# Performance work log

Hardware: AMD Instinct MI355X
Metric: run time of the kernel (lower is better)

The kernel has to match this reference:

```python
import jax, jax.numpy as jnp
import numpy as np
import math

BS, L, DIM, H = 2, 1024, 1024, 16
DPH = DIM // H            # 64 dim per head
PHI_DIM = DPH * 1         # phi_size_ratio = 1
N_PROJS = 200
MIN_LOG_STD = math.log(1e-5)
SQRT_PHI = math.sqrt(PHI_DIM)


def setup_inputs() -> dict:
    key = jax.random.key(0)
    ks = jax.random.split(key, 8)
    lin = lambda k: jax.random.normal(k, (DIM, DIM), jnp.float32) * 0.02
    return {
        "x": jax.random.normal(ks[0], (BS, L, DIM), jnp.float32),
        "mask": jnp.ones((BS, L), dtype=jnp.bool_),
        "Wq": lin(ks[1]), "bq": jnp.zeros((DIM,), jnp.float32),
        "Wk": lin(ks[2]), "bk": jnp.zeros((DIM,), jnp.float32),
        "Wv": lin(ks[3]), "bv": jnp.zeros((DIM,), jnp.float32),
        "Wo": lin(ks[4]), "bo": jnp.zeros((DIM,), jnp.float32),
        "log_sigma": jnp.zeros((H, 1, DPH), jnp.float32),  # log(1.0) init
        "random_projs": jax.random.normal(ks[5], (N_PROJS, PHI_DIM, DPH), jnp.float32),
    }


def _phi(x, rp_scaled):
    # x: (b, l, h, d); rp_scaled: (h, phi, d). arccos features: relu(proj) / sqrt(phi_dim)
    x = x / jnp.maximum(jnp.linalg.norm(x, axis=-1, keepdims=True), 1e-12)
    px = jnp.einsum('blhd,hpd->blhp', x, rp_scaled)
    return jax.nn.relu(px) / SQRT_PHI


def _causal_rfa(phi_q, phi_k, v):
    # sequential S,z recurrence, time-major scan
    def step(carry, inp):
        S, z = carry
        pk, pq, vt = inp                       # (b,h,phi),(b,h,phi),(b,h,d)
        S = S + pk[..., :, None] * vt[..., None, :]
        z = z + pk
        num = jnp.einsum('bhp,bhpd->bhd', pq, S)
        den = jnp.einsum('bhp,bhp->bh', pq, z)
        return (S, z), num / jnp.maximum(den, 1e-5)[..., None]

    S0 = jnp.zeros((BS, H, PHI_DIM, DPH), jnp.float32)
    z0 = jnp.zeros((BS, H, PHI_DIM), jnp.float32)
    xs = (jnp.transpose(phi_k, (1, 0, 2, 3)),
          jnp.transpose(phi_q, (1, 0, 2, 3)),
          jnp.transpose(v, (1, 0, 2, 3)))
    _, h_t = jax.lax.scan(step, (S0, z0), xs)  # (l, b, h, d)
    return jnp.transpose(h_t, (1, 0, 2, 3))     # (b, l, h, d)


def reference(x, mask, Wq, bq, Wk, bk, Wv, bv, Wo, bo, log_sigma, random_projs):
    q = (x @ Wq.T + bq).reshape(BS, L, H, DPH)
    k = (x @ Wk.T + bk).reshape(BS, L, H, DPH)
    v = (x @ Wv.T + bv).reshape(BS, L, H, DPH)
    # eval mode: proj_id = 0 for every head
    scale = jnp.exp(jnp.maximum(log_sigma, MIN_LOG_STD))                  # (h,1,d)
    rp = scale * jnp.broadcast_to(random_projs[0], (H, PHI_DIM, DPH))     # (h,phi,d)
    phi_q = _phi(q, rp)
    phi_k = _phi(k, rp) * mask[:, :, None, None].astype(jnp.float32)
    h = _causal_rfa(phi_q, phi_k, v)                                      # (b,l,h,d)
    return h.reshape(BS, L, DIM) @ Wo.T + bo
```

## Files before the change

### kernel.cpp

```cpp
#include <hip/hip_runtime.h>


typedef unsigned short ushort_t;
typedef unsigned long long u64_t;
typedef __attribute__((ext_vector_type(8))) __bf16 bf16x8;
typedef __attribute__((ext_vector_type(4))) float f32x4;

#define MLS -11.512925464970229f

__device__ __forceinline__ ushort_t f2b(float f) {
  union { float f; unsigned u; } v; v.f = f;
  unsigned r = v.u + 0x7FFFu + ((v.u >> 16) & 1u);
  return (ushort_t)(r >> 16);
}

__device__ __forceinline__ void gload16(const void* g, void* l) {
  __builtin_amdgcn_global_load_lds((__attribute__((address_space(1))) void*)(void*)g,
                                   (__attribute__((address_space(3))) void*)l, 16, 0, 0);
}

__device__ __forceinline__ f32x4 mfma_bf16(bf16x8 a, bf16x8 b, f32x4 c) {
  return __builtin_amdgcn_mfma_f32_16x16x32_bf16(a, b, c, 0, 0, 0);
}

__global__ __launch_bounds__(256) void convert_kernel(
    const float* __restrict__ x, const float* __restrict__ Wq, const float* __restrict__ Wk,
    const float* __restrict__ Wv, const float* __restrict__ Wo,
    const float* __restrict__ bq, const float* __restrict__ bk, const float* __restrict__ bv,
    const float* __restrict__ lsig, const float* __restrict__ rp0,
    ushort_t* __restrict__ xb, ushort_t* __restrict__ Wcat, ushort_t* __restrict__ Wob,
    float* __restrict__ bcat, float* __restrict__ sclbuf, ushort_t* __restrict__ rpb) {
  const size_t NX = (size_t)1 << 21, NW = (size_t)1 << 20;
  const size_t nch = (NX + 4 * NW) >> 3;
  size_t stride = (size_t)gridDim.x * 256;
  for (size_t i = (size_t)blockIdx.x * 256 + threadIdx.x; i < nch + 1024; i += stride) {
    if (i < nch) {
      size_t e = i << 3;
      const float* src; ushort_t* dst;
      if (e < NX)            { src = x  + e;               dst = xb   + e; }
      else if (e < NX + NW)  { src = Wq + (e - NX);        dst = Wcat + (e - NX); }
      else if (e < NX + 2*NW){ src = Wk + (e - NX - NW);   dst = Wcat + (e - NX); }
      else if (e < NX + 3*NW){ src = Wv + (e - NX - 2*NW); dst = Wcat + (e - NX); }
      else                   { src = Wo + (e - NX - 3*NW); dst = Wob  + (e - NX - 3*NW); }
      float4 a = *(const float4*)src, c = *(const float4*)(src + 4);
      uint4 u;
      u.x = (unsigned)f2b(a.x) | ((unsigned)f2b(a.y) << 16);
      u.y = (unsigned)f2b(a.z) | ((unsigned)f2b(a.w) << 16);
      u.z = (unsigned)f2b(c.x) | ((unsigned)f2b(c.y) << 16);
      u.w = (unsigned)f2b(c.z) | ((unsigned)f2b(c.w) << 16);
      *(uint4*)dst = u;
    } else {
      int j = (int)(i - nch);
      sclbuf[j] = expf(fmaxf(lsig[j], MLS));
      bcat[j] = bq[j]; bcat[1024 + j] = bk[j]; bcat[2048 + j] = bv[j];
#pragma unroll
      for (int jj = 0; jj < 4; ++jj) {
        int pe = j * 4 + jj;
        rpb[pe] = f2b(rp0[pe]);
      }
    }
  }
}

__global__ __launch_bounds__(512, 2) void qkvphi_kernel(
    const ushort_t* __restrict__ A, const ushort_t* __restrict__ Bm,
    const float* __restrict__ bias, const float* __restrict__ sclbuf,
    const ushort_t* __restrict__ rpb,
    ushort_t* __restrict__ phiq, ushort_t* __restrict__ phik, ushort_t* __restrict__ vbT,
    float* __restrict__ Sg, float* __restrict__ zg) {
  __shared__ __align__(16) ushort_t smem[40960];
  const int K = 1024;
  int blk = blockIdx.x;
  int hg = blk & 15, by = blk >> 4;
  int m0 = by << 7;
  int tid = threadIdx.x;
  int w = tid >> 6, l = tid & 63;
  int wr = w & 3, wc = w >> 2;
  int lr = l & 15, lg = l >> 4;
  bf16x8 rpf[2][4];
#pragma unroll
  for (int kk = 0; kk < 2; ++kk)
#pragma unroll
    for (int ni = 0; ni < 4; ++ni)
      rpf[kk][ni] = *(const bf16x8*)(rpb + (ni*16 + lr)*64 + kk*32 + lg*8);

  f32x4 acc[2][6] = {};
  auto stage = [&](int buf, int k0) {
    ushort_t* Ad = smem + buf*8192;
    ushort_t* Bd = smem + 16384 + buf*12288;
#pragma unroll
    for (int it = 0; it < 2; ++it) {
      int idx = it*512 + tid, row = idx >> 3, cg = idx & 7;
      gload16(A + (size_t)(m0 + row)*K + k0 + ((cg ^ (row & 7)) << 3), Ad + idx*8);
    }
#pragma unroll
    for (int it = 0; it < 3; ++it) {
      int idx = it*512 + tid, row = idx >> 3, cg = idx & 7;
      int grow = (row >> 6)*1024 + hg*64 + (row & 63);
      gload16(Bm + (size_t)grow*K + k0 + ((cg ^ (row & 7)) << 3), Bd + idx*8);
    }
  };
  auto compute = [&](int buf) {
    const ushort_t* Ab = smem + buf*8192;
    const ushort_t* Bb = smem + 16384 + buf*12288;
#pragma unroll
    for (int kk = 0; kk < 2; ++kk) {
      bf16x8 af[2], bfr[6];
#pragma unroll
      for (int ii = 0; ii < 2; ++ii) {
        int r = wr*32 + ii*16 + lr;
        af[ii] = *(const bf16x8*)(Ab + r*64 + (((kk*4 + lg) ^ (r & 7)) << 3));
      }
#pragma unroll
      for (int ii = 0; ii < 6; ++ii) {
        int brow = (ii < 4) ? (wc*64 + ii*16 + lr) : (128 + wc*32 + (ii - 4)*16 + lr);
        bfr[ii] = *(const bf16x8*)(Bb + brow*64 + (((kk*4 + lg) ^ (brow & 7)) << 3));
      }
#pragma unroll
      for (int mi = 0; mi < 2; ++mi)
#pragma unroll
        for (int ni = 0; ni < 6; ++ni)
          acc[mi][ni] = mfma_bf16(af[mi], bfr[ni], acc[mi][ni]);
    }
  };
  stage(0, 0);
  for (int t = 0; t < 15; ++t) {
    stage((t + 1) & 1, (t + 1) * 64);
    asm volatile("s_waitcnt vmcnt(5)" ::: "memory");
    __builtin_amdgcn_s_barrier();
    compute(t & 1);
    asm volatile("s_waitcnt lgkmcnt(0)" ::: "memory");
    __builtin_amdgcn_s_barrier();
  }
  asm volatile("s_waitcnt vmcnt(0)" ::: "memory");
  __builtin_amdgcn_s_barrier();
  compute(1);
  __syncthreads();

  int b = m0 >> 10, tloc0 = m0 & 1023;
  int kt = tloc0 >> 7;
  size_t hbase = ((size_t)(b*16 + hg) << 16);
  {
    ushort_t* Vt = smem + 16384;
    float bv2[2];
#pragma unroll
    for (int j = 0; j < 2; ++j) bv2[j] = bias[2048 + hg*64 + wc*32 + j*16 + lr];
#pragma unroll
    for (int mi = 0; mi < 2; ++mi) {
      int lloc0 = wr*32 + mi*16 + lg*4;
#pragma unroll
      for (int j = 0; j < 2; ++j) {
        int d = wc*32 + j*16 + lr;
        u64_t u = 0;
#pragma unroll
        for (int r = 0; r < 4; ++r)
          u |= (u64_t)f2b(acc[mi][4 + j][r] + bv2[j]) << (16*r);
        int sv0 = (lloc0 & 7) | ((((lloc0 >> 3) ^ (d & 15)) & 15) << 3);
        *(u64_t*)(Vt + d*128 + sv0) = u;
      }
    }
  }
  ushort_t* Ys = smem + w*2048;
  {
    float bias4[4], scl4[4];
#pragma unroll
    for (int ni = 0; ni < 4; ++ni) {
      bias4[ni] = bias[wc*1024 + hg*64 + ni*16 + lr];
      scl4[ni]  = sclbuf[hg*64 + ni*16 + lr];
    }
#pragma unroll
    for (int mi = 0; mi < 2; ++mi) {
      float v4[4][4];
      float ss[4] = {0.f, 0.f, 0.f, 0.f};
#pragma unroll
      for (int ni = 0; ni < 4; ++ni)
#pragma unroll
        for (int r = 0; r < 4; ++r) {
          float vv = acc[mi][ni][r] + bias4[ni];
          v4[ni][r] = vv;
          ss[r] += vv * vv;
        }
#pragma unroll
      for (int r = 0; r < 4; ++r) {
        float s = ss[r];
        s += __shfl_xor(s, 1); s += __shfl_xor(s, 2);
        s += __shfl_xor(s, 4); s += __shfl_xor(s, 8);
        ss[r] = 1.f / fmaxf(sqrtf(s), 1e-12f);
      }
#pragma unroll
      for (int ni = 0; ni < 4; ++ni) {
        int c = ni*16 + lr;
#pragma unroll
        for (int r = 0; r < 4; ++r) {
          int rl = mi*16 + lg*4 + r;
          Ys[rl*64 + (((c >> 3) ^ (rl & 7)) << 3) + (c & 7)] = f2b(v4[ni][r] * ss[r] * scl4[ni]);
        }
      }
    }
  }
  {
    ushort_t* dst = wc ? phik : phiq;
    ushort_t* KT = smem + 28672;
    float* zpart = (float*)(smem + 36864);
    f32x4 acc2[2][4] = {};
#pragma unroll
    for (int kk = 0; kk < 2; ++kk) {
      bf16x8 af2[2];
#pragma unroll
      for (int mi = 0; mi < 2; ++mi) {
        int rl = mi*16 + lr;
        af2[mi] = *(const bf16x8*)(Ys + rl*64 + (((kk*4 + lg) ^ (rl & 7)) << 3));
      }
#pragma unroll
      for (int mi = 0; mi < 2; ++mi)
#pragma unroll
        for (int ni = 0; ni < 4; ++ni)
          acc2[mi][ni] = mfma_bf16(af2[mi], rpf[kk][ni], acc2[mi][ni]);
    }
    ushort_t* Pt = Ys;
    float zp[4] = {0.f, 0.f, 0.f, 0.f};
#pragma unroll
    for (int mi = 0; mi < 2; ++mi)
#pragma unroll
      for (int ni = 0; ni < 4; ++ni) {
        u64_t ku = 0;
#pragma unroll
        for (int r = 0; r < 4; ++r) {
          int rl = mi*16 + lg*4 + r;
          int p = ni*16 + lr;
          float val = fmaxf(acc2[mi][ni][r], 0.f) * 0.125f;
          ushort_t uv = f2b(val);
          int sp = (p & 7) | ((((p >> 3) ^ (rl & 7)) & 7) << 3);
          Pt[rl*64 + sp] = uv;
          ku |= (u64_t)uv << (16*r);
          zp[ni] += val;
        }
        if (wc) {
          int lloc0 = wr*32 + mi*16 + lg*4;
          int p = ni*16 + lr;
          int sv0 = (lloc0 & 7) | ((((lloc0 >> 3) ^ (p & 15)) & 15) << 3);
          *(u64_t*)(KT + p*128 + sv0) = ku;
        }
      }
    if (wc) {
#pragma unroll
      for (int ni = 0; ni < 4; ++ni) {
        float s = zp[ni];
        s += __shfl_xor(s, 16); s += __shfl_xor(s, 32);
        if (lg == 0) zpart[wr*64 + ni*16 + lr] = s;
      }
    }
    size_t gp = hbase + (size_t)(tloc0 + wr*32)*64;
#pragma unroll
    for (int ii = 0; ii < 4; ++ii) {
      int chunk = ii*64 + l;
      uint4 u = *(const uint4*)(Pt + chunk*8);
      *(uint4*)(dst + gp + chunk*8) = u;
    }
  }
  __syncthreads();
  if (wc == 0) {
    const ushort_t* Vt = smem + 16384;
    const ushort_t* KT = smem + 28672;
    f32x4 sacc[4] = {};
#pragma unroll
    for (int kk = 0; kk < 4; ++kk) {
      int p = wr*16 + lr;
      bf16x8 af = *(const bf16x8*)(KT + p*128 + (((kk*4 + lg) ^ (p & 15)) << 3));
#pragma unroll
      for (int ni = 0; ni < 4; ++ni) {
        int d = ni*16 + lr;
        bf16x8 bfv = *(const bf16x8*)(Vt + d*128 + (((kk*4 + lg) ^ (d & 15)) << 3));
        sacc[ni] = mfma_bf16(af, bfv, sacc[ni]);
      }
    }
    float* Sb = Sg + (((size_t)(b*16 + hg))*8 + kt)*4096;
#pragma unroll
    for (int ni = 0; ni < 4; ++ni)
#pragma unroll
      for (int r = 0; r < 4; ++r)
        Sb[(wr*16 + lg*4 + r)*64 + ni*16 + lr] = sacc[ni][r];
  } else if (w == 4) {
    const float* zpart = (const float*)(smem + 36864);
    float s = zpart[l & 63] + zpart[64 + (l & 63)] + zpart[128 + (l & 63)] + zpart[192 + (l & 63)];
    zg[(((size_t)(b*16 + hg))*8 + kt)*64 + (l & 63)] = s;
  }
  {
    const ushort_t* Vt = smem + 16384;
#pragma unroll
    for (int c = tid; c < 1024; c += 512) {
      int d = c >> 4, off = c & 15;
      uint4 u = *(const uint4*)(Vt + c*8);
      *(uint4*)(vbT + hbase + (size_t)d*1024 + kt*128 + off*8) = u;
    }
  }
}

__global__ __launch_bounds__(256) void outproj_kernel(
    const ushort_t* __restrict__ A, const ushort_t* __restrict__ Bm,
    const float* __restrict__ bias, float* __restrict__ C) {
  __shared__ __align__(16) ushort_t smem[16384];
  const int K = 1024;
  int wid = (blockIdx.x & 7) * 64 + (blockIdx.x >> 3);
  int bx = wid & 15, by = wid >> 4;
  int m0 = by << 6, n0 = bx << 6;
  int tid = threadIdx.x, w = tid >> 6, l = tid & 63;
  int lr = l & 15, lg = l >> 4;
  auto stage = [&](int buf, int k0) {
    ushort_t* Ad = smem + buf*4096;
    ushort_t* Bd = smem + 8192 + buf*4096;
#pragma unroll
    for (int it = 0; it < 2; ++it) {
      int idx = it*256 + tid, row = idx >> 3, cg = idx & 7;
      gload16(A + (size_t)(m0 + row)*K + k0 + ((cg ^ (row & 7)) << 3), Ad + idx*8);
    }
#pragma unroll
    for (int it = 0; it < 2; ++it) {
      int idx = it*256 + tid, row = idx >> 3, cg = idx & 7;
      gload16(Bm + (size_t)(n0 + row)*K + k0 + ((cg ^ (row & 7)) << 3), Bd + idx*8);
    }
  };
  f32x4 acc[4] = {};
  auto compute = [&](int buf) {
    const ushort_t* Ab = smem + buf*4096;
    const ushort_t* Bb = smem + 8192 + buf*4096;
#pragma unroll
    for (int kk = 0; kk < 2; ++kk) {
      int ra = w*16 + lr;
      bf16x8 af = *(const bf16x8*)(Ab + ra*64 + (((kk*4 + lg) ^ (ra & 7)) << 3));
      bf16x8 bfr[4];
#pragma unroll
      for (int i = 0; i < 4; ++i) {
        int rb = i*16 + lr;
        bfr[i] = *(const bf16x8*)(Bb + rb*64 + (((kk*4 + lg) ^ (rb & 7)) << 3));
      }
#pragma unroll
      for (int ni = 0; ni < 4; ++ni)
        acc[ni] = mfma_bf16(af, bfr[ni], acc[ni]);
    }
  };
  stage(0, 0);
  for (int t = 0; t < 15; ++t) {
    stage((t + 1) & 1, (t + 1) * 64);
    asm volatile("s_waitcnt vmcnt(4)" ::: "memory");
    __builtin_amdgcn_s_barrier();
    compute(t & 1);
    asm volatile("s_waitcnt lgkmcnt(0)" ::: "memory");
    __builtin_amdgcn_s_barrier();
  }
  asm volatile("s_waitcnt vmcnt(0)" ::: "memory");
  __builtin_amdgcn_s_barrier();
  compute(1);
#pragma unroll
  for (int ni = 0; ni < 4; ++ni) {
    int col = n0 + ni*16 + lr;
    float bv = bias[col];
#pragma unroll
    for (int r = 0; r < 4; ++r)
      C[(size_t)(m0 + w*16 + lg*4 + r)*1024 + col] = acc[ni][r] + bv;
  }
}

__global__ __launch_bounds__(256) void attn_kernel(
    const ushort_t* __restrict__ phiq, const ushort_t* __restrict__ phik,
    const ushort_t* __restrict__ vbT, const float* __restrict__ Sg,
    const float* __restrict__ zg, ushort_t* __restrict__ hb) {
  __shared__ __align__(16) ushort_t smem[46336];
  ushort_t* Qs  = smem;
  ushort_t* Ks  = smem + 8192;
  ushort_t* Vs  = smem + 16384;
  ushort_t* Ps  = smem + 24576;
  ushort_t* SpT = smem + 40960;
  float* den_lds = (float*)(smem + 46080);
  int blk = blockIdx.x;
  int qt = blk >> 5, bh = blk & 31;
  int b = bh >> 4, h = bh & 15;
  int tid = threadIdx.x, w = tid >> 6, l = tid & 63;
  int lr = l & 15, lg = l >> 4;
  const ushort_t* pq = phiq + ((size_t)bh << 16) + qt*8192;
  const ushort_t* pk = phik + ((size_t)bh << 16) + qt*8192;
  const ushort_t* pv = vbT  + ((size_t)bh << 16);
#pragma unroll
  for (int it = 0; it < 4; ++it) { int idx = it*256 + tid; gload16(pq + idx*8, Qs + idx*8); }
#pragma unroll
  for (int it = 0; it < 4; ++it) { int idx = it*256 + tid; gload16(pk + idx*8, Ks + idx*8); }
#pragma unroll
  for (int it = 0; it < 4; ++it) {
    int idx = it*256 + tid;
    gload16(pv + (idx >> 4)*1024 + qt*128 + (idx & 15)*8, Vs + idx*8);
  }
  f32x4 nacc[2][4] = {};
  f32x4 dcr[2] = {};
  if (qt > 0) {
    f32x4 s4[4] = {};
    const float* Sb = Sg + ((size_t)bh * 8) * 4096;
    for (int kt = 0; kt < qt; ++kt) {
#pragma unroll
      for (int i = 0; i < 4; ++i)
        s4[i] += *(const f32x4*)(Sb + kt*4096 + tid*16 + i*4);
    }
    float zz = 0.f;
    if (tid < 64) {
      for (int kt = 0; kt < qt; ++kt) zz += zg[((size_t)bh*8 + kt)*64 + tid];
    }
    for (int i = tid; i < 960; i += 256) SpT[4160 + i] = 0;
#pragma unroll
    for (int i = 0; i < 4; ++i)
#pragma unroll
      for (int c = 0; c < 4; ++c) {
        int e = tid*16 + i*4 + c;
        int p = e >> 6, d = e & 63;
        SpT[d*64 + ((((p >> 3) ^ (d & 7)) & 7) << 3) + (p & 7)] = f2b(s4[i][c]);
      }
    if (tid < 64) SpT[4096 + tid] = f2b(zz);
    asm volatile("s_waitcnt vmcnt(8) lgkmcnt(0)" ::: "memory");
    __builtin_amdgcn_s_barrier();
#pragma unroll
    for (int kk = 0; kk < 2; ++kk) {
      bf16x8 af[2], bfv[5];
#pragma unroll
      for (int qi = 0; qi < 2; ++qi) {
        int q = w*32 + qi*16 + lr;
        af[qi] = *(const bf16x8*)(Qs + q*64 + (((kk*4 + lg) ^ (q & 7)) << 3));
      }
#pragma unroll
      for (int ni = 0; ni < 5; ++ni) {
        int rr = ni*16 + lr;
        bfv[ni] = *(const bf16x8*)(SpT + rr*64 + (((kk*4 + lg) ^ (rr & 7)) << 3));
      }
#pragma unroll
      for (int qi = 0; qi < 2; ++qi) {
#pragma unroll
        for (int ni = 0; ni < 4; ++ni)
          nacc[qi][ni] = mfma_bf16(af[qi], bfv[ni], nacc[qi][ni]);
        dcr[qi] = mfma_bf16(af[qi], bfv[4], dcr[qi]);
      }
    }
  }
  asm volatile("s_waitcnt vmcnt(0)" ::: "memory");
  __builtin_amdgcn_s_barrier();
  float den[2] = {0.f, 0.f};
  {
    bf16x8 qf[2][2];
#pragma unroll
    for (int qi = 0; qi < 2; ++qi)
#pragma unroll
      for (int ks = 0; ks < 2; ++ks) {
        int q = w*32 + qi*16 + lr;
        qf[qi][ks] = *(const bf16x8*)(Qs + q*64 + (((ks*4 + lg) ^ (q & 7)) << 3));
      }
    f32x4 sfr[8][2] = {};
#pragma unroll
    for (int kf = 0; kf < 8; ++kf)
#pragma unroll
      for (int ks = 0; ks < 2; ++ks) {
        int kloc = kf*16 + lr;
        bf16x8 af = *(const bf16x8*)(Ks + kloc*64 + (((ks*4 + lg) ^ (kloc & 7)) << 3));
        sfr[kf][0] = mfma_bf16(af, qf[0][ks], sfr[kf][0]);
        sfr[kf][1] = mfma_bf16(af, qf[1][ks], sfr[kf][1]);
      }
#pragma unroll
    for (int kf = 0; kf < 8; ++kf)
#pragma unroll
      for (int qi = 0; qi < 2; ++qi) {
        int q = w*32 + qi*16 + lr;
        f32x4 v4 = sfr[kf][qi];
        int keyb = kf*16 + lg*4;
#pragma unroll
        for (int r = 0; r < 4; ++r)
          if (keyb + r > q) v4[r] = 0.f;
        den[qi] += v4[0] + v4[1] + v4[2] + v4[3];
        unsigned lo, hi;
        asm("v_cvt_pk_bf16_f32 %0, %1, %2" : "=v"(lo) : "v"(v4[0]), "v"(v4[1]));
        asm("v_cvt_pk_bf16_f32 %0, %1, %2" : "=v"(hi) : "v"(v4[2]), "v"(v4[3]));
        int chunk = (2*kf + (lg >> 1)) ^ (q & 7);
        uint2 u; u.x = lo; u.y = hi;
        *(uint2*)(Ps + q*128 + chunk*8 + (lg & 1)*4) = u;
      }
#pragma unroll
    for (int ks = 0; ks < 4; ++ks) {
      bf16x8 pa[2];
#pragma unroll
      for (int qi = 0; qi < 2; ++qi) {
        int q = w*32 + qi*16 + lr;
        pa[qi] = *(const bf16x8*)(Ps + q*128 + (((4*ks + lg) ^ (q & 7)) << 3));
      }
#pragma unroll
      for (int df = 0; df < 4; ++df) {
        int d = df*16 + lr;
        bf16x8 vf = *(const bf16x8*)(Vs + d*128 + (((4*ks + lg) ^ (d & 15)) << 3));
        nacc[0][df] = mfma_bf16(pa[0], vf, nacc[0][df]);
        nacc[1][df] = mfma_bf16(pa[1], vf, nacc[1][df]);
      }
    }
  }
  den[0] += __shfl_xor(den[0], 16); den[0] += __shfl_xor(den[0], 32);
  den[1] += __shfl_xor(den[1], 16); den[1] += __shfl_xor(den[1], 32);
  if (lg == 0) {
    den_lds[w*32 + lr]      = den[0];
    den_lds[w*32 + 16 + lr] = den[1];
  }
  __syncthreads();
  if (qt > 0 && lr == 0) {
#pragma unroll
    for (int qi = 0; qi < 2; ++qi)
#pragma unroll
      for (int r = 0; r < 4; ++r)
        den_lds[w*32 + qi*16 + lg*4 + r] += dcr[qi][r];
  }
  __syncthreads();
#pragma unroll
  for (int qi = 0; qi < 2; ++qi)
#pragma unroll
    for (int df = 0; df < 4; ++df)
#pragma unroll
      for (int r = 0; r < 4; ++r) {
        int qloc = w*32 + qi*16 + lg*4 + r;
        int d = df*16 + lr;
        float dd = fmaxf(den_lds[qloc], 1e-5f);
        hb[((size_t)(b*1024 + qt*128 + qloc))*1024 + h*64 + d] = f2b(nacc[qi][df][r] / dd);
      }
}

extern "C" void kernel_launch(void* const* d_in, const int* in_sizes, int n_in,
                              void* d_out, int out_size, void* d_ws, size_t ws_size,
                              hipStream_t stream) {
  const float* x  = (const float*)d_in[0];
  const float* Wq = (const float*)d_in[2];
  const float* bq = (const float*)d_in[3];
  const float* Wk = (const float*)d_in[4];
  const float* bk = (const float*)d_in[5];
  const float* Wv = (const float*)d_in[6];
  const float* bv = (const float*)d_in[7];
  const float* Wo = (const float*)d_in[8];
  const float* bo = (const float*)d_in[9];
  const float* ls = (const float*)d_in[10];
  const float* rp = (const float*)d_in[11];

  char* ws = (char*)d_ws;
  size_t off = 0;
  auto alloc = [&](size_t bytes) { char* p = ws + off; off += (bytes + 255) & ~(size_t)255; return p; };
  ushort_t* xb     = (ushort_t*)alloc((size_t)2048*1024*2);
  ushort_t* Wcat   = (ushort_t*)alloc((size_t)3072*1024*2);
  ushort_t* Wob    = (ushort_t*)alloc((size_t)1024*1024*2);
  float*    bcat   = (float*)   alloc((size_t)3072*4);
  float*    sclbuf = (float*)   alloc((size_t)1024*4);
  ushort_t* rpb    = (ushort_t*)alloc((size_t)64*64*2);
  ushort_t* phiq   = (ushort_t*)alloc((size_t)32*1024*64*2);
  ushort_t* phik   = (ushort_t*)alloc((size_t)32*1024*64*2);
  ushort_t* vbT    = (ushort_t*)alloc((size_t)32*64*1024*2);
  ushort_t* hb     = (ushort_t*)alloc((size_t)2048*1024*2);
  float*    Sg     = (float*)   alloc((size_t)32*8*4096*4);
  float*    zg     = (float*)   alloc((size_t)32*8*64*4);

  convert_kernel<<<1024, 256, 0, stream>>>(x, Wq, Wk, Wv, Wo, bq, bk, bv, ls, rp,
                                           xb, Wcat, Wob, bcat, sclbuf, rpb);
  qkvphi_kernel<<<256, 512, 0, stream>>>(xb, Wcat, bcat, sclbuf, rpb, phiq, phik, vbT, Sg, zg);
  attn_kernel<<<256, 256, 0, stream>>>(phiq, phik, vbT, Sg, zg, hb);
  outproj_kernel<<<512, 256, 0, stream>>>(hb, Wob, bo, (float*)d_out);
}
```

Baseline: 53.83 us.

## Triple-buffer QKV GEMM main loop with interleaved loads and MFMA priority

Moves the fused QKV projection GEMM from a double-buffered to a triple-buffered LDS pipeline with a prefetch distance of two. Each k-step is split into four MFMA phases, with the B-tile global loads interleaved between them and s_setprio raised around the MFMA bursts. The random-projection fragments are now loaded after the GEMM instead of before it, which lowers register pressure during the main loop. The cost is more LDS per block (about 120 KB instead of 80 KB), which may lower occupancy below the two blocks per CU the launch bounds target, plus many more barriers per iteration.

```diff
diff --git a/kernel.cpp b/kernel.cpp
--- a/kernel.cpp
+++ b/kernel.cpp
@@ -68,7 +68,7 @@
     const ushort_t* __restrict__ rpb,
     ushort_t* __restrict__ phiq, ushort_t* __restrict__ phik, ushort_t* __restrict__ vbT,
     float* __restrict__ Sg, float* __restrict__ zg) {
-  __shared__ __align__(16) ushort_t smem[40960];
+  __shared__ __align__(16) ushort_t smem[61440];
   const int K = 1024;
   int blk = blockIdx.x;
   int hg = blk & 15, by = blk >> 4;
@@ -77,64 +77,103 @@
   int w = tid >> 6, l = tid & 63;
   int wr = w & 3, wc = w >> 2;
   int lr = l & 15, lg = l >> 4;
-  bf16x8 rpf[2][4];
-#pragma unroll
-  for (int kk = 0; kk < 2; ++kk)
-#pragma unroll
-    for (int ni = 0; ni < 4; ++ni)
-      rpf[kk][ni] = *(const bf16x8*)(rpb + (ni*16 + lr)*64 + kk*32 + lg*8);
 
   f32x4 acc[2][6] = {};
-  auto stage = [&](int buf, int k0) {
+  auto sA = [&](int buf, int k0) {
     ushort_t* Ad = smem + buf*8192;
-    ushort_t* Bd = smem + 16384 + buf*12288;
 #pragma unroll
     for (int it = 0; it < 2; ++it) {
       int idx = it*512 + tid, row = idx >> 3, cg = idx & 7;
       gload16(A + (size_t)(m0 + row)*K + k0 + ((cg ^ (row & 7)) << 3), Ad + idx*8);
     }
-#pragma unroll
-    for (int it = 0; it < 3; ++it) {
-      int idx = it*512 + tid, row = idx >> 3, cg = idx & 7;
-      int grow = (row >> 6)*1024 + hg*64 + (row & 63);
-      gload16(Bm + (size_t)grow*K + k0 + ((cg ^ (row & 7)) << 3), Bd + idx*8);
-    }
   };
-  auto compute = [&](int buf) {
+  auto sB = [&](int buf, int k0, int part) {
+    ushort_t* Bd = smem + 24576 + buf*12288;
+    int idx = part*512 + tid, row = idx >> 3, cg = idx & 7;
+    int grow = (row >> 6)*1024 + hg*64 + (row & 63);
+    gload16(Bm + (size_t)grow*K + k0 + ((cg ^ (row & 7)) << 3), Bd + idx*8);
+  };
+  auto rdA = [&](int buf, int kk, bf16x8* af) {
     const ushort_t* Ab = smem + buf*8192;
-    const ushort_t* Bb = smem + 16384 + buf*12288;
-#pragma unroll
-    for (int kk = 0; kk < 2; ++kk) {
-      bf16x8 af[2], bfr[6];
-#pragma unroll
-      for (int ii = 0; ii < 2; ++ii) {
-        int r = wr*32 + ii*16 + lr;
-        af[ii] = *(const bf16x8*)(Ab + r*64 + (((kk*4 + lg) ^ (r & 7)) << 3));
-      }
-#pragma unroll
-      for (int ii = 0; ii < 6; ++ii) {
-        int brow = (ii < 4) ? (wc*64 + ii*16 + lr) : (128 + wc*32 + (ii - 4)*16 + lr);
-        bfr[ii] = *(const bf16x8*)(Bb + brow*64 + (((kk*4 + lg) ^ (brow & 7)) << 3));
-      }
-#pragma unroll
-      for (int mi = 0; mi < 2; ++mi)
-#pragma unroll
-        for (int ni = 0; ni < 6; ++ni)
-          acc[mi][ni] = mfma_bf16(af[mi], bfr[ni], acc[mi][ni]);
+#pragma unroll
+    for (int ii = 0; ii < 2; ++ii) {
+      int r = wr*32 + ii*16 + lr;
+      af[ii] = *(const bf16x8*)(Ab + r*64 + (((kk*4 + lg) ^ (r & 7)) << 3));
     }
   };
-  stage(0, 0);
-  for (int t = 0; t < 15; ++t) {
-    stage((t + 1) & 1, (t + 1) * 64);
-    asm volatile("s_waitcnt vmcnt(5)" ::: "memory");
-    __builtin_amdgcn_s_barrier();
-    compute(t & 1);
+  auto rdB = [&](int buf, int kk, int ni0, bf16x8* b3) {
+    const ushort_t* Bb = smem + 24576 + buf*12288;
+#pragma unroll
+    for (int ii = 0; ii < 3; ++ii) {
+      int i = ni0 + ii;
+      int brow = (i < 4) ? (wc*64 + i*16 + lr) : (128 + wc*32 + (i - 4)*16 + lr);
+      b3[ii] = *(const bf16x8*)(Bb + brow*64 + (((kk*4 + lg) ^ (brow & 7)) << 3));
+    }
+  };
+  sA(0, 0);  sB(0, 0, 0);  sB(0, 0, 1);  sB(0, 0, 2);
+  sA(1, 64); sB(1, 64, 0); sB(1, 64, 1); sB(1, 64, 2);
+  for (int t = 0; t < 16; ++t) {
+    int cur = t % 3, nx2 = (t + 2) % 3;
+    bool pf = t < 14;
+    int k2 = (t + 2) * 64;
+    bf16x8 af0[2], af1[2], b0[3], b1[3];
+    if (pf) {
+      sA(nx2, k2);
+      asm volatile("s_waitcnt vmcnt(7)" ::: "memory");
+    } else if (t == 14) {
+      asm volatile("s_waitcnt vmcnt(5)" ::: "memory");
+    } else {
+      asm volatile("s_waitcnt vmcnt(0)" ::: "memory");
+    }
+    __builtin_amdgcn_s_barrier();
+    rdA(cur, 0, af0);
+    rdB(cur, 0, 0, b0);
     asm volatile("s_waitcnt lgkmcnt(0)" ::: "memory");
-    __builtin_amdgcn_s_barrier();
-  }
-  asm volatile("s_waitcnt vmcnt(0)" ::: "memory");
-  __builtin_amdgcn_s_barrier();
-  compute(1);
+    __builtin_amdgcn_s_setprio(1);
+#pragma unroll
+    for (int j = 0; j < 3; ++j) {
+      acc[0][j] = mfma_bf16(af0[0], b0[j], acc[0][j]);
+      acc[1][j] = mfma_bf16(af0[1], b0[j], acc[1][j]);
+    }
+    __builtin_amdgcn_s_setprio(0);
+    __builtin_amdgcn_s_barrier();
+    rdB(cur, 0, 3, b1);
+    if (pf) { sB(nx2, k2, 0); sB(nx2, k2, 1); }
+    __builtin_amdgcn_s_barrier();
+    asm volatile("s_waitcnt lgkmcnt(0)" ::: "memory");
+    __builtin_amdgcn_s_setprio(1);
+#pragma unroll
+    for (int j = 0; j < 3; ++j) {
+      acc[0][3 + j] = mfma_bf16(af0[0], b1[j], acc[0][3 + j]);
+      acc[1][3 + j] = mfma_bf16(af0[1], b1[j], acc[1][3 + j]);
+    }
+    __builtin_amdgcn_s_setprio(0);
+    __builtin_amdgcn_s_barrier();
+    rdA(cur, 1, af1);
+    rdB(cur, 1, 0, b0);
+    if (pf) sB(nx2, k2, 2);
+    __builtin_amdgcn_s_barrier();
+    asm volatile("s_waitcnt lgkmcnt(0)" ::: "memory");
+    __builtin_amdgcn_s_setprio(1);
+#pragma unroll
+    for (int j = 0; j < 3; ++j) {
+      acc[0][j] = mfma_bf16(af1[0], b0[j], acc[0][j]);
+      acc[1][j] = mfma_bf16(af1[1], b0[j], acc[1][j]);
+    }
+    __builtin_amdgcn_s_setprio(0);
+    __builtin_amdgcn_s_barrier();
+    rdB(cur, 1, 3, b1);
+    __builtin_amdgcn_s_barrier();
+    asm volatile("s_waitcnt lgkmcnt(0)" ::: "memory");
+    __builtin_amdgcn_s_setprio(1);
+#pragma unroll
+    for (int j = 0; j < 3; ++j) {
+      acc[0][3 + j] = mfma_bf16(af1[0], b1[j], acc[0][3 + j]);
+      acc[1][3 + j] = mfma_bf16(af1[1], b1[j], acc[1][3 + j]);
+    }
+    __builtin_amdgcn_s_setprio(0);
+    __builtin_amdgcn_s_barrier();
+  }
   __syncthreads();
 
   int b = m0 >> 10, tloc0 = m0 & 1023;
@@ -199,6 +238,12 @@
     }
   }
   {
+    bf16x8 rpf[2][4];
+#pragma unroll
+    for (int kk = 0; kk < 2; ++kk)
+#pragma unroll
+      for (int ni = 0; ni < 4; ++ni)
+        rpf[kk][ni] = *(const bf16x8*)(rpb + (ni*16 + lr)*64 + kk*32 + lg*8);
     ushort_t* dst = wc ? phik : phiq;
     ushort_t* KT = smem + 28672;
     float* zpart = (float*)(smem + 36864);
```

Result: slower. 55.63 us (+3.3%).
